# Kernel optimization log

Measured on AMD Instinct MI355X. Metric: run time of the kernel, lower is better.

Reference implementation:

```python
import jax, jax.numpy as jnp
import numpy as np

NUM_HEADS = 8
HEAD_CH = 32  # embed_channels // num_heads = 256 // 8
BN_EPS = 1e-3


def _conv(x, w, pad):
    return jax.lax.conv_general_dilated(
        x, w, window_strides=(1, 1), padding=[(pad, pad), (pad, pad)],
        dimension_numbers=('NCHW', 'OIHW', 'NCHW'))


def _bn(x, gamma, beta):
    # inference BN with running_mean=0, running_var=1 (fresh buffers)
    scale = gamma / jnp.sqrt(1.0 + BN_EPS)
    return x * scale[None, :, None, None] + beta[None, :, None, None]


def setup_inputs() -> dict:
    key = jax.random.key(0)
    ks = jax.random.split(key, 8)
    B, Cin, H, W = 16, 512, 40, 40
    N, Cg, E, Cout = 80, 512, 256, 512
    s = 0.05
    return {
        'x': jax.random.normal(ks[0], (B, Cin, H, W), jnp.float32),
        'guide': jax.random.normal(ks[1], (B, N, Cg), jnp.float32),
        'We': jax.random.normal(ks[2], (E, Cin, 1, 1), jnp.float32) * s,
        'gamma_e': jnp.ones((E,), jnp.float32),
        'beta_e': jnp.zeros((E,), jnp.float32),
        'Wg': jax.random.normal(ks[3], (E, Cg), jnp.float32) * s,
        'bg': jnp.zeros((E,), jnp.float32),
        'head_bias': jnp.zeros((NUM_HEADS,), jnp.float32),
        'Wp': jax.random.normal(ks[4], (Cout, Cin, 3, 3), jnp.float32) * s,
        'gamma_p': jnp.ones((Cout,), jnp.float32),
        'beta_p': jnp.zeros((Cout,), jnp.float32),
    }


def reference(x, guide, We, gamma_e, beta_e, Wg, bg, head_bias, Wp, gamma_p, beta_p):
    B, _, H, W = x.shape
    M, C = NUM_HEADS, HEAD_CH
    # guide_fc: [B, n, Cg] -> [B, n, M, C]
    g = (jnp.einsum('bnc,ec->bne', guide, Wg) + bg).reshape(B, -1, M, C)
    # embed_conv (1x1 + BN, no act): [B, M, C, H, W]
    e = _bn(_conv(x, We, 0), gamma_e, beta_e).reshape(B, M, C, H, W)
    # attention scores, max over guide tokens, scale, bias, sigmoid
    attn = jnp.einsum('bmchw,bnmc->bmhwn', e, g)
    attn = jnp.max(attn, axis=-1) / (C ** 0.5)
    attn = jax.nn.sigmoid(attn + head_bias[None, :, None, None])
    # project_conv (3x3 + BN, no act), gated per head
    p = _bn(_conv(x, Wp, 1), gamma_p, beta_p)
    p = p.reshape(B, M, -1, H, W) * attn[:, :, None, :, :]
    return p.reshape(B, -1, H, W)
```

## Files before the change

kernel.cpp:

```cpp
#include <hip/hip_runtime.h>
#include <hip/hip_bf16.h>
#include <stdint.h>

#define B_   16
#define CIN  512
#define HW   1600
#define E_   256
#define NTOK 80
#define CG   512
#define COUT 512
#define NHEAD 8
#define HCH  32
#define SP   (42*42)

typedef __attribute__((ext_vector_type(8))) short bf16x8;
typedef __attribute__((ext_vector_type(4))) float f32x4;

__device__ __forceinline__ unsigned short f2bf(float f) {
  union { float f; unsigned int i; } v; v.f = f;
  unsigned int x = v.i;
  return (unsigned short)((x + 0x7FFFu + ((x >> 16) & 1u)) >> 16);
}

__global__ void k_prep_x(const float* __restrict__ x, unsigned short* __restrict__ xt) {
  __shared__ float tile[32][33];
  int hw0 = blockIdx.x * 32, ci0 = blockIdx.y * 32, b = blockIdx.z;
  int tx = threadIdx.x, ty = threadIdx.y;
  const float* xp = x + ((size_t)b * CIN + ci0) * HW + hw0;
#pragma unroll
  for (int j = 0; j < 4; j++) tile[ty + 8 * j][tx] = xp[(size_t)(ty + 8 * j) * HW + tx];
  __syncthreads();
  int ci = ci0 + tx;
#pragma unroll
  for (int j = 0; j < 4; j++) {
    int hw = hw0 + ty + 8 * j;
    int h = hw / 40, w = hw - h * 40;
    xt[((size_t)b * SP + (size_t)(h + 1) * 42 + (w + 1)) * CIN + ci] = f2bf(tile[tx][ty + 8 * j]);
  }
}

__global__ void k_prep_wp(const float* __restrict__ Wp, unsigned short* __restrict__ wpb2) {
  int idx = blockIdx.x * 256 + threadIdx.x;
  int co = idx >> 9, ci = idx & 511;
  const float* s = Wp + (size_t)idx * 9;
#pragma unroll
  for (int t = 0; t < 9; t++) wpb2[(size_t)co * (9 * CIN) + t * CIN + ci] = f2bf(s[t]);
}

__global__ void k_cast_all(const float* __restrict__ We, unsigned short* __restrict__ web,
                           const float* __restrict__ Wg, unsigned short* __restrict__ wgb,
                           const float* __restrict__ gu, unsigned short* __restrict__ gub) {
  int i = blockIdx.x * 256 + threadIdx.x;
  const float* src; unsigned short* dst; int j;
  if (i < 32768)       { src = We; dst = web; j = i; }
  else if (i < 65536)  { src = Wg; dst = wgb; j = i - 32768; }
  else                 { src = gu; dst = gub; j = i - 65536; }
  float4 v = ((const float4*)src)[j];
  ushort4 o; o.x = f2bf(v.x); o.y = f2bf(v.y); o.z = f2bf(v.z); o.w = f2bf(v.w);
  ((ushort4*)dst)[j] = o;
}

__global__ __launch_bounds__(512, 2)
void k_fused(const unsigned short* __restrict__ wpb2, const unsigned short* __restrict__ web,
             const unsigned short* __restrict__ wgb,  const unsigned short* __restrict__ xt,
             const unsigned short* __restrict__ gub,
             const float* __restrict__ gamma_e, const float* __restrict__ beta_e,
             const float* __restrict__ gamma_p, const float* __restrict__ beta_p,
             const float* __restrict__ bg,
             float* __restrict__ out, unsigned short* __restrict__ et,
             unsigned short* __restrict__ gbf) {
  __shared__ unsigned short L[3 * 16384];
  char* LB = (char*)L;
  int tid = threadIdx.x;
  int wg = blockIdx.x;

  int role, m0, n0;
  if (wg < 200)      { int w = (wg & 7) * 25 + (wg >> 3);
                       role = 0; m0 = (w / 100) * 256; n0 = (w % 100) * 256; }
  else if (wg < 300) { role = 1; m0 = 0; n0 = (wg - 200) * 256; }
  else               { role = 2; m0 = 0; n0 = (wg - 300) * 256; }

  const int RS    = (role == 0) ? 9 * CIN : CIN;
  const int NSTEP = (role == 0) ? 144 : 16;
  const bool tapjump = (role == 0);
  const unsigned short* Aw = (role == 0) ? wpb2 : (role == 1) ? web : wgb;

  int lane = tid & 63, wid = tid >> 6;
  int wr = wid >> 2, wc = wid & 3;

  int rloc = tid >> 2;
  int kq_g = ((tid & 3) ^ ((tid >> 3) & 3)) * 8;
  const unsigned short* pA = Aw + (size_t)(m0 + rloc) * RS + kq_g;
  const unsigned short* pB0;
  const unsigned short* pB1;
  if (role == 2) {
    pB0 = gub + (size_t)(n0 + rloc) * CIN + kq_g;
    pB1 = pB0 + (size_t)128 * CIN;
  } else {
    int c0 = n0 + rloc, c1 = c0 + 128;
    int b0 = c0 / 1600, hw0 = c0 - b0 * 1600;
    int b1 = c1 / 1600, hw1 = c1 - b1 * 1600;
    int h0 = hw0 / 40, w0 = hw0 - h0 * 40;
    int h1 = hw1 / 40, w1 = hw1 - h1 * 40;
    int ctr = (role == 1) ? 43 : 0;
    pB0 = xt + ((size_t)b0 * SP + h0 * 42 + w0 + ctr) * CIN + kq_g;
    pB1 = xt + ((size_t)b1 * SP + h1 * 42 + w1 + ctr) * CIN + kq_g;
  }

  int scnt = 0;
#define GL(src, dst) __builtin_amdgcn_global_load_lds((const __attribute__((address_space(1))) unsigned int*)(src), \
        (__attribute__((address_space(3))) unsigned int*)(dst), 16, 0, 0)
  auto STG_A = [&](unsigned bo) {
    GL(pA,            LB + bo +     0u + tid * 16u);
    GL(pA + 128 * RS, LB + bo +  8192u + tid * 16u);
  };
  auto STG_B = [&](unsigned bo) {
    GL(pB0,           LB + bo + 16384u + tid * 16u);
    GL(pB1,           LB + bo + 24576u + tid * 16u);
  };
  auto ADV = [&]() {
    pA += 32; pB0 += 32; pB1 += 32;
    if (tapjump) { ++scnt; if ((scnt % 48) == 0) { pB0 += 19968; pB1 += 19968; } }
  };

  int frow = lane & 15;
  int sg = ((lane >> 4) ^ ((frow >> 1) & 3)) << 4;
  int aoff[8], boff[4];
#pragma unroll
  for (int i = 0; i < 8; i++) aoff[i] = (wr * 128 + i * 16 + frow) * 64 + sg;
#pragma unroll
  for (int i = 0; i < 4; i++) boff[i] = 16384 + (wc * 64 + i * 16 + frow) * 64 + sg;

  f32x4 acc[8][4] = {};

  STG_A(0u); STG_B(0u); ADV();
  STG_A(32768u); STG_B(32768u); ADV();
  unsigned r0 = 0u, r1 = 32768u, r2 = 65536u;

  for (int s = 0; s < NSTEP; ++s) {
    if (s + 1 < NSTEP) { asm volatile("s_waitcnt vmcnt(4)" ::: "memory"); }
    else               { asm volatile("s_waitcnt vmcnt(0)" ::: "memory"); }
    __builtin_amdgcn_s_barrier();
    __builtin_amdgcn_sched_barrier(0);
    const char* base = LB + r0;
    bool pre = (s + 2 < NSTEP);
    bf16x8 af[8], bv[4];
#pragma unroll
    for (int i = 0; i < 4; i++) af[i] = *(const bf16x8*)(base + aoff[i]);
#pragma unroll
    for (int i = 0; i < 4; i++) bv[i] = *(const bf16x8*)(base + boff[i]);
    if (pre) STG_A(r2);
    __builtin_amdgcn_s_barrier();
    __builtin_amdgcn_s_setprio(1);
#pragma unroll
    for (int mi = 0; mi < 4; mi++)
#pragma unroll
      for (int ni = 0; ni < 4; ni++)
        acc[mi][ni] = __builtin_amdgcn_mfma_f32_16x16x32_bf16(af[mi], bv[ni], acc[mi][ni], 0, 0, 0);
    __builtin_amdgcn_s_setprio(0);
    __builtin_amdgcn_s_barrier();
#pragma unroll
    for (int i = 4; i < 8; i++) af[i] = *(const bf16x8*)(base + aoff[i]);
    if (pre) { STG_B(r2); ADV(); }
    __builtin_amdgcn_s_barrier();
    __builtin_amdgcn_s_setprio(1);
#pragma unroll
    for (int mi = 4; mi < 8; mi++)
#pragma unroll
      for (int ni = 0; ni < 4; ni++)
        acc[mi][ni] = __builtin_amdgcn_mfma_f32_16x16x32_bf16(af[mi], bv[ni], acc[mi][ni], 0, 0, 0);
    __builtin_amdgcn_s_setprio(0);
    unsigned t = r0; r0 = r1; r1 = r2; r2 = t;
  }
#undef GL

  const float BN_RSQ = 0.9995003746877732f;
  int colb = n0 + wc * 64 + frow;
  int rowb = m0 + wr * 128 + (lane >> 4) * 4;
  if (role == 0) {
#pragma unroll
    for (int mi = 0; mi < 8; mi++) {
      float sc[4], bt[4];
#pragma unroll
      for (int j = 0; j < 4; j++) {
        int co = rowb + mi * 16 + j;
        sc[j] = gamma_p[co] * BN_RSQ; bt[j] = beta_p[co];
      }
#pragma unroll
      for (int ni = 0; ni < 4; ni++) {
        int col = colb + ni * 16;
        int b = col / 1600, hw = col - b * 1600;
#pragma unroll
        for (int j = 0; j < 4; j++) {
          int co = rowb + mi * 16 + j;
          out[((size_t)b * COUT + co) * HW + hw] = acc[mi][ni][j] * sc[j] + bt[j];
        }
      }
    }
  } else if (role == 1) {
#pragma unroll
    for (int mi = 0; mi < 8; mi++) {
      float sc[4], bt[4];
#pragma unroll
      for (int j = 0; j < 4; j++) {
        int ech = rowb + mi * 16 + j;
        sc[j] = gamma_e[ech] * BN_RSQ; bt[j] = beta_e[ech];
      }
#pragma unroll
      for (int ni = 0; ni < 4; ni++) {
        int col = colb + ni * 16;
        int b = col / 1600, hw = col - b * 1600;
        ushort4 pk;
        pk.x = f2bf(acc[mi][ni][0] * sc[0] + bt[0]);
        pk.y = f2bf(acc[mi][ni][1] * sc[1] + bt[1]);
        pk.z = f2bf(acc[mi][ni][2] * sc[2] + bt[2]);
        pk.w = f2bf(acc[mi][ni][3] * sc[3] + bt[3]);
        *(ushort4*)(et + ((size_t)b * HW + hw) * E_ + (rowb + mi * 16)) = pk;
      }
    }
  } else {
#pragma unroll
    for (int mi = 0; mi < 8; mi++) {
      float bt[4];
#pragma unroll
      for (int j = 0; j < 4; j++) bt[j] = bg[rowb + mi * 16 + j];
#pragma unroll
      for (int ni = 0; ni < 4; ni++) {
        int col = colb + ni * 16;
        ushort4 pk;
        pk.x = f2bf(acc[mi][ni][0] + bt[0]);
        pk.y = f2bf(acc[mi][ni][1] + bt[1]);
        pk.z = f2bf(acc[mi][ni][2] + bt[2]);
        pk.w = f2bf(acc[mi][ni][3] + bt[3]);
        *(ushort4*)(gbf + (size_t)col * E_ + (rowb + mi * 16)) = pk;
      }
    }
  }
}

__global__ void k_attn_mfma(const unsigned short* __restrict__ et, const unsigned short* __restrict__ gbf,
                            const float* __restrict__ head_bias, float* __restrict__ attn) {
  __shared__ unsigned short gs[NTOK * HCH];
  int b = blockIdx.z, m = blockIdx.y;
  int tid = threadIdx.x, lane = tid & 63, wid = tid >> 6;
  for (int i = tid; i < NTOK * HCH / 8; i += 256) {
    int n = i >> 2, c = (i & 3) * 8;
    *(bf16x8*)&gs[n * HCH + c] = *(const bf16x8*)&gbf[((size_t)b * NTOK + n) * E_ + m * HCH + c];
  }
  __syncthreads();
  int col = lane & 15, kq = (lane >> 4) * 8;
  bf16x8 bfr[5];
#pragma unroll
  for (int ni = 0; ni < 5; ni++)
    bfr[ni] = *(const bf16x8*)&gs[(ni * 16 + col) * HCH + kq];

  int hw0 = blockIdx.x * 256 + wid * 64;
  bf16x8 afr[4];
#pragma unroll
  for (int mi = 0; mi < 4; mi++) {
    int hw = hw0 + mi * 16 + col; if (hw > HW - 1) hw = HW - 1;
    afr[mi] = *(const bf16x8*)&et[((size_t)b * HW + hw) * E_ + m * HCH + kq];
  }
  float hb = head_bias[m];
  float* attnp = attn + ((size_t)b * NHEAD + m) * HW;
#pragma unroll
  for (int mi = 0; mi < 4; mi++) {
    f32x4 d[5];
#pragma unroll
    for (int ni = 0; ni < 5; ni++) {
      f32x4 z = {0.f, 0.f, 0.f, 0.f};
      d[ni] = __builtin_amdgcn_mfma_f32_16x16x32_bf16(afr[mi], bfr[ni], z, 0, 0, 0);
    }
#pragma unroll
    for (int j = 0; j < 4; j++) {
      float v = fmaxf(fmaxf(fmaxf(d[0][j], d[1][j]), fmaxf(d[2][j], d[3][j])), d[4][j]);
      v = fmaxf(v, __shfl_xor(v, 1, 16));
      v = fmaxf(v, __shfl_xor(v, 2, 16));
      v = fmaxf(v, __shfl_xor(v, 4, 16));
      v = fmaxf(v, __shfl_xor(v, 8, 16));
      if (col == j) {
        int hwout = hw0 + mi * 16 + (lane >> 4) * 4 + j;
        if (hwout < HW)
          attnp[hwout] = 1.0f / (1.0f + __expf(-(v * 0.17677669529663687f + hb)));
      }
    }
  }
}

__global__ void k_gate(float* __restrict__ out, const float* __restrict__ attn) {
  int idx = blockIdx.x * 256 + threadIdx.x;
  int f4 = idx * 4;
  int b = f4 / (COUT * HW);
  int rem = f4 - b * (COUT * HW);
  int co = rem / HW, hw = rem - co * HW;
  float4 a = *(const float4*)(attn + ((size_t)b * NHEAD + (co >> 6)) * HW + hw);
  float4 p = ((float4*)out)[idx];
  p.x *= a.x; p.y *= a.y; p.z *= a.z; p.w *= a.w;
  ((float4*)out)[idx] = p;
}

extern "C" void kernel_launch(void* const* d_in, const int* in_sizes, int n_in,
                              void* d_out, int out_size, void* d_ws, size_t ws_size,
                              hipStream_t stream) {
  const float* x         = (const float*)d_in[0];
  const float* guide     = (const float*)d_in[1];
  const float* We        = (const float*)d_in[2];
  const float* gamma_e   = (const float*)d_in[3];
  const float* beta_e    = (const float*)d_in[4];
  const float* Wg        = (const float*)d_in[5];
  const float* bg        = (const float*)d_in[6];
  const float* head_bias = (const float*)d_in[7];
  const float* Wp        = (const float*)d_in[8];
  const float* gamma_p   = (const float*)d_in[9];
  const float* beta_p    = (const float*)d_in[10];
  float* out = (float*)d_out;

  char* ws = (char*)d_ws;
  size_t off = 0;
  auto alloc = [&](size_t bytes) { char* p = ws + off; off += (bytes + 255) & ~(size_t)255; return p; };
  unsigned short* xt   = (unsigned short*)alloc((size_t)B_ * SP * CIN * 2);
  unsigned short* wpb2 = (unsigned short*)alloc((size_t)COUT * 9 * CIN * 2);
  unsigned short* web  = (unsigned short*)alloc((size_t)E_ * CIN * 2);
  unsigned short* wgb  = (unsigned short*)alloc((size_t)E_ * CG * 2);
  unsigned short* gub  = (unsigned short*)alloc((size_t)B_ * NTOK * CG * 2);
  unsigned short* gbf  = (unsigned short*)alloc((size_t)B_ * NTOK * E_ * 2);
  unsigned short* et   = (unsigned short*)alloc((size_t)B_ * HW * E_ * 2);
  float* attn          = (float*)alloc((size_t)B_ * NHEAD * HW * 4);

  hipMemsetAsync(xt, 0, (size_t)B_ * SP * CIN * 2, stream);
  k_prep_x<<<dim3(50, 16, B_), dim3(32, 8), 0, stream>>>(x, xt);
  k_prep_wp<<<dim3(1024), dim3(256), 0, stream>>>(Wp, wpb2);
  k_cast_all<<<dim3(896), dim3(256), 0, stream>>>(We, web, Wg, wgb, guide, gub);
  k_fused<<<dim3(305), dim3(512), 0, stream>>>(wpb2, web, wgb, xt, gub,
      gamma_e, beta_e, gamma_p, beta_p, bg, out, et, gbf);
  k_attn_mfma<<<dim3(7, NHEAD, B_), dim3(256), 0, stream>>>(et, gbf, head_bias, attn);
  k_gate<<<dim3(12800), dim3(256), 0, stream>>>(out, attn);
}
```

Measured before the change: 302.1 us.

## Split fused GEMM into stages and fuse attention gate into conv epilogue

```diff
diff --git a/kernel.cpp b/kernel.cpp
--- a/kernel.cpp
+++ b/kernel.cpp
@@ -37,14 +37,6 @@
     int h = hw / 40, w = hw - h * 40;
     xt[((size_t)b * SP + (size_t)(h + 1) * 42 + (w + 1)) * CIN + ci] = f2bf(tile[tx][ty + 8 * j]);
   }
-}
-
-__global__ void k_prep_wp(const float* __restrict__ Wp, unsigned short* __restrict__ wpb2) {
-  int idx = blockIdx.x * 256 + threadIdx.x;
-  int co = idx >> 9, ci = idx & 511;
-  const float* s = Wp + (size_t)idx * 9;
-#pragma unroll
-  for (int t = 0; t < 9; t++) wpb2[(size_t)co * (9 * CIN) + t * CIN + ci] = f2bf(s[t]);
 }
 
 __global__ void k_cast_all(const float* __restrict__ We, unsigned short* __restrict__ web,
@@ -60,31 +52,16 @@
   ((ushort4*)dst)[j] = o;
 }
 
-__global__ __launch_bounds__(512, 2)
-void k_fused(const unsigned short* __restrict__ wpb2, const unsigned short* __restrict__ web,
-             const unsigned short* __restrict__ wgb,  const unsigned short* __restrict__ xt,
-             const unsigned short* __restrict__ gub,
-             const float* __restrict__ gamma_e, const float* __restrict__ beta_e,
-             const float* __restrict__ gamma_p, const float* __restrict__ beta_p,
-             const float* __restrict__ bg,
-             float* __restrict__ out, unsigned short* __restrict__ et,
-             unsigned short* __restrict__ gbf) {
-  __shared__ unsigned short L[3 * 16384];
-  char* LB = (char*)L;
+template<int EPI>
+__device__ __forceinline__ void gemm_body(
+    const unsigned short* __restrict__ Aw, const unsigned short* __restrict__ Bx,
+    int m0, int n0,
+    const float* __restrict__ g_sc, const float* __restrict__ g_bt,
+    const float* __restrict__ attn, float* __restrict__ out,
+    unsigned short* __restrict__ ob16, char* LB) {
+  constexpr int RS    = (EPI == 1) ? 9 * CIN : CIN;
+  constexpr int NSTEP = (EPI == 1) ? 144 : 16;
   int tid = threadIdx.x;
-  int wg = blockIdx.x;
-
-  int role, m0, n0;
-  if (wg < 200)      { int w = (wg & 7) * 25 + (wg >> 3);
-                       role = 0; m0 = (w / 100) * 256; n0 = (w % 100) * 256; }
-  else if (wg < 300) { role = 1; m0 = 0; n0 = (wg - 200) * 256; }
-  else               { role = 2; m0 = 0; n0 = (wg - 300) * 256; }
-
-  const int RS    = (role == 0) ? 9 * CIN : CIN;
-  const int NSTEP = (role == 0) ? 144 : 16;
-  const bool tapjump = (role == 0);
-  const unsigned short* Aw = (role == 0) ? wpb2 : (role == 1) ? web : wgb;
-
   int lane = tid & 63, wid = tid >> 6;
   int wr = wid >> 2, wc = wid & 3;
 
@@ -93,8 +70,8 @@
   const unsigned short* pA = Aw + (size_t)(m0 + rloc) * RS + kq_g;
   const unsigned short* pB0;
   const unsigned short* pB1;
-  if (role == 2) {
-    pB0 = gub + (size_t)(n0 + rloc) * CIN + kq_g;
+  if constexpr (EPI == 2) {
+    pB0 = Bx + (size_t)(n0 + rloc) * CIN + kq_g;
     pB1 = pB0 + (size_t)128 * CIN;
   } else {
     int c0 = n0 + rloc, c1 = c0 + 128;
@@ -102,25 +79,24 @@
     int b1 = c1 / 1600, hw1 = c1 - b1 * 1600;
     int h0 = hw0 / 40, w0 = hw0 - h0 * 40;
     int h1 = hw1 / 40, w1 = hw1 - h1 * 40;
-    int ctr = (role == 1) ? 43 : 0;
-    pB0 = xt + ((size_t)b0 * SP + h0 * 42 + w0 + ctr) * CIN + kq_g;
-    pB1 = xt + ((size_t)b1 * SP + h1 * 42 + w1 + ctr) * CIN + kq_g;
+    constexpr int ctr = (EPI == 0) ? 43 : 0;
+    pB0 = Bx + ((size_t)b0 * SP + h0 * 42 + w0 + ctr) * CIN + kq_g;
+    pB1 = Bx + ((size_t)b1 * SP + h1 * 42 + w1 + ctr) * CIN + kq_g;
   }
 
   int scnt = 0;
 #define GL(src, dst) __builtin_amdgcn_global_load_lds((const __attribute__((address_space(1))) unsigned int*)(src), \
         (__attribute__((address_space(3))) unsigned int*)(dst), 16, 0, 0)
-  auto STG_A = [&](unsigned bo) {
+  auto STG = [&](unsigned bo) {
     GL(pA,            LB + bo +     0u + tid * 16u);
     GL(pA + 128 * RS, LB + bo +  8192u + tid * 16u);
-  };
-  auto STG_B = [&](unsigned bo) {
     GL(pB0,           LB + bo + 16384u + tid * 16u);
     GL(pB1,           LB + bo + 24576u + tid * 16u);
-  };
-  auto ADV = [&]() {
     pA += 32; pB0 += 32; pB1 += 32;
-    if (tapjump) { ++scnt; if ((scnt % 48) == 0) { pB0 += 19968; pB1 += 19968; } }
+    if constexpr (EPI == 1) {
+      ++scnt;
+      if ((scnt % 48) == 0) { pB0 += 19968; pB1 += 19968; }
+    }
   };
 
   int frow = lane & 15;
@@ -133,43 +109,61 @@
 
   f32x4 acc[8][4] = {};
 
-  STG_A(0u); STG_B(0u); ADV();
-  STG_A(32768u); STG_B(32768u); ADV();
+  STG(0u); STG(32768u);
   unsigned r0 = 0u, r1 = 32768u, r2 = 65536u;
-
   for (int s = 0; s < NSTEP; ++s) {
     if (s + 1 < NSTEP) { asm volatile("s_waitcnt vmcnt(4)" ::: "memory"); }
     else               { asm volatile("s_waitcnt vmcnt(0)" ::: "memory"); }
     __builtin_amdgcn_s_barrier();
     __builtin_amdgcn_sched_barrier(0);
+    if (s + 2 < NSTEP) STG(r2);
     const char* base = LB + r0;
-    bool pre = (s + 2 < NSTEP);
-    bf16x8 af[8], bv[4];
-#pragma unroll
-    for (int i = 0; i < 4; i++) af[i] = *(const bf16x8*)(base + aoff[i]);
+    bf16x8 bv[4];
 #pragma unroll
     for (int i = 0; i < 4; i++) bv[i] = *(const bf16x8*)(base + boff[i]);
-    if (pre) STG_A(r2);
-    __builtin_amdgcn_s_barrier();
-    __builtin_amdgcn_s_setprio(1);
-#pragma unroll
-    for (int mi = 0; mi < 4; mi++)
-#pragma unroll
-      for (int ni = 0; ni < 4; ni++)
-        acc[mi][ni] = __builtin_amdgcn_mfma_f32_16x16x32_bf16(af[mi], bv[ni], acc[mi][ni], 0, 0, 0);
-    __builtin_amdgcn_s_setprio(0);
-    __builtin_amdgcn_s_barrier();
-#pragma unroll
-    for (int i = 4; i < 8; i++) af[i] = *(const bf16x8*)(base + aoff[i]);
-    if (pre) { STG_B(r2); ADV(); }
-    __builtin_amdgcn_s_barrier();
-    __builtin_amdgcn_s_setprio(1);
-#pragma unroll
-    for (int mi = 4; mi < 8; mi++)
-#pragma unroll
-      for (int ni = 0; ni < 4; ni++)
-        acc[mi][ni] = __builtin_amdgcn_mfma_f32_16x16x32_bf16(af[mi], bv[ni], acc[mi][ni], 0, 0, 0);
-    __builtin_amdgcn_s_setprio(0);
+    if ((wid & 1) == 0) {
+      bf16x8 a0[4];
+#pragma unroll
+      for (int i = 0; i < 4; i++) a0[i] = *(const bf16x8*)(base + aoff[i]);
+      __builtin_amdgcn_s_setprio(1);
+#pragma unroll
+      for (int mi = 0; mi < 4; mi++)
+#pragma unroll
+        for (int ni = 0; ni < 4; ni++)
+          acc[mi][ni] = __builtin_amdgcn_mfma_f32_16x16x32_bf16(a0[mi], bv[ni], acc[mi][ni], 0, 0, 0);
+      __builtin_amdgcn_s_setprio(0);
+      bf16x8 a1[4];
+#pragma unroll
+      for (int i = 0; i < 4; i++) a1[i] = *(const bf16x8*)(base + aoff[4 + i]);
+      __builtin_amdgcn_s_setprio(1);
+#pragma unroll
+      for (int mi = 0; mi < 4; mi++)
+#pragma unroll
+        for (int ni = 0; ni < 4; ni++)
+          acc[4 + mi][ni] = __builtin_amdgcn_mfma_f32_16x16x32_bf16(a1[mi], bv[ni], acc[4 + mi][ni], 0, 0, 0);
+      __builtin_amdgcn_s_setprio(0);
+    } else {
+      bf16x8 a1[4];
+#pragma unroll
+      for (int i = 0; i < 4; i++) a1[i] = *(const bf16x8*)(base + aoff[4 + i]);
+      __builtin_amdgcn_s_setprio(1);
+#pragma unroll
+      for (int mi = 0; mi < 4; mi++)
+#pragma unroll
+        for (int ni = 0; ni < 4; ni++)
+          acc[4 + mi][ni] = __builtin_amdgcn_mfma_f32_16x16x32_bf16(a1[mi], bv[ni], acc[4 + mi][ni], 0, 0, 0);
+      __builtin_amdgcn_s_setprio(0);
+      bf16x8 a0[4];
+#pragma unroll
+      for (int i = 0; i < 4; i++) a0[i] = *(const bf16x8*)(base + aoff[i]);
+      __builtin_amdgcn_s_setprio(1);
+#pragma unroll
+      for (int mi = 0; mi < 4; mi++)
+#pragma unroll
+        for (int ni = 0; ni < 4; ni++)
+          acc[mi][ni] = __builtin_amdgcn_mfma_f32_16x16x32_bf16(a0[mi], bv[ni], acc[mi][ni], 0, 0, 0);
+      __builtin_amdgcn_s_setprio(0);
+    }
     unsigned t = r0; r0 = r1; r1 = r2; r2 = t;
   }
 #undef GL
@@ -177,34 +171,36 @@
   const float BN_RSQ = 0.9995003746877732f;
   int colb = n0 + wc * 64 + frow;
   int rowb = m0 + wr * 128 + (lane >> 4) * 4;
-  if (role == 0) {
+  if constexpr (EPI == 1) {
 #pragma unroll
     for (int mi = 0; mi < 8; mi++) {
+      int head = (m0 + wr * 128 + mi * 16) >> 6;
       float sc[4], bt[4];
 #pragma unroll
       for (int j = 0; j < 4; j++) {
         int co = rowb + mi * 16 + j;
-        sc[j] = gamma_p[co] * BN_RSQ; bt[j] = beta_p[co];
+        sc[j] = g_sc[co] * BN_RSQ; bt[j] = g_bt[co];
       }
 #pragma unroll
       for (int ni = 0; ni < 4; ni++) {
         int col = colb + ni * 16;
         int b = col / 1600, hw = col - b * 1600;
+        float gate = attn[((size_t)b * NHEAD + head) * HW + hw];
 #pragma unroll
         for (int j = 0; j < 4; j++) {
           int co = rowb + mi * 16 + j;
-          out[((size_t)b * COUT + co) * HW + hw] = acc[mi][ni][j] * sc[j] + bt[j];
+          out[((size_t)b * COUT + co) * HW + hw] = (acc[mi][ni][j] * sc[j] + bt[j]) * gate;
         }
       }
     }
-  } else if (role == 1) {
+  } else if constexpr (EPI == 0) {
 #pragma unroll
     for (int mi = 0; mi < 8; mi++) {
       float sc[4], bt[4];
 #pragma unroll
       for (int j = 0; j < 4; j++) {
         int ech = rowb + mi * 16 + j;
-        sc[j] = gamma_e[ech] * BN_RSQ; bt[j] = beta_e[ech];
+        sc[j] = g_sc[ech] * BN_RSQ; bt[j] = g_bt[ech];
       }
 #pragma unroll
       for (int ni = 0; ni < 4; ni++) {
@@ -215,7 +211,7 @@
         pk.y = f2bf(acc[mi][ni][1] * sc[1] + bt[1]);
         pk.z = f2bf(acc[mi][ni][2] * sc[2] + bt[2]);
         pk.w = f2bf(acc[mi][ni][3] * sc[3] + bt[3]);
-        *(ushort4*)(et + ((size_t)b * HW + hw) * E_ + (rowb + mi * 16)) = pk;
+        *(ushort4*)(ob16 + ((size_t)b * HW + hw) * E_ + (rowb + mi * 16)) = pk;
       }
     }
   } else {
@@ -223,7 +219,7 @@
     for (int mi = 0; mi < 8; mi++) {
       float bt[4];
 #pragma unroll
-      for (int j = 0; j < 4; j++) bt[j] = bg[rowb + mi * 16 + j];
+      for (int j = 0; j < 4; j++) bt[j] = g_bt[rowb + mi * 16 + j];
 #pragma unroll
       for (int ni = 0; ni < 4; ni++) {
         int col = colb + ni * 16;
@@ -232,10 +228,45 @@
         pk.y = f2bf(acc[mi][ni][1] + bt[1]);
         pk.z = f2bf(acc[mi][ni][2] + bt[2]);
         pk.w = f2bf(acc[mi][ni][3] + bt[3]);
-        *(ushort4*)(gbf + (size_t)col * E_ + (rowb + mi * 16)) = pk;
-      }
-    }
-  }
+        *(ushort4*)(ob16 + (size_t)col * E_ + (rowb + mi * 16)) = pk;
+      }
+    }
+  }
+}
+
+__global__ __launch_bounds__(512, 1)
+void k_stage1(const unsigned short* __restrict__ web, const unsigned short* __restrict__ wgb,
+              const unsigned short* __restrict__ xt,  const unsigned short* __restrict__ gub,
+              const float* __restrict__ gamma_e, const float* __restrict__ beta_e,
+              const float* __restrict__ bg,
+              unsigned short* __restrict__ et, unsigned short* __restrict__ gbf,
+              const float* __restrict__ Wp, unsigned short* __restrict__ wpb2) {
+  __shared__ unsigned short L[3 * 16384];
+  int wg = blockIdx.x;
+  if (wg < 100) {
+    gemm_body<0>(web, xt, 0, wg * 256, gamma_e, beta_e, nullptr, nullptr, et, (char*)L);
+  } else if (wg < 105) {
+    gemm_body<2>(wgb, gub, 0, (wg - 100) * 256, nullptr, bg, nullptr, nullptr, gbf, (char*)L);
+  } else {
+    int g = (wg - 105) * 512 + threadIdx.x;
+    for (int idx = g; idx < COUT * CIN; idx += 150 * 512) {
+      int co = idx >> 9, ci = idx & 511;
+      const float* s = Wp + (size_t)idx * 9;
+#pragma unroll
+      for (int t = 0; t < 9; t++) wpb2[(size_t)co * (9 * CIN) + t * CIN + ci] = f2bf(s[t]);
+    }
+  }
+}
+
+__global__ __launch_bounds__(512, 1)
+void k_conv3(const unsigned short* __restrict__ wpb2, const unsigned short* __restrict__ xt,
+             const float* __restrict__ gamma_p, const float* __restrict__ beta_p,
+             const float* __restrict__ attn, float* __restrict__ out) {
+  __shared__ unsigned short L[3 * 16384];
+  int wg = blockIdx.x;
+  int w = (wg & 7) * 25 + (wg >> 3);
+  int m0 = (w / 100) * 256, n0 = (w % 100) * 256;
+  gemm_body<1>(wpb2, xt, m0, n0, gamma_p, beta_p, attn, out, nullptr, (char*)L);
 }
 
 __global__ void k_attn_mfma(const unsigned short* __restrict__ et, const unsigned short* __restrict__ gbf,
@@ -285,18 +316,6 @@
       }
     }
   }
-}
-
-__global__ void k_gate(float* __restrict__ out, const float* __restrict__ attn) {
-  int idx = blockIdx.x * 256 + threadIdx.x;
-  int f4 = idx * 4;
-  int b = f4 / (COUT * HW);
-  int rem = f4 - b * (COUT * HW);
-  int co = rem / HW, hw = rem - co * HW;
-  float4 a = *(const float4*)(attn + ((size_t)b * NHEAD + (co >> 6)) * HW + hw);
-  float4 p = ((float4*)out)[idx];
-  p.x *= a.x; p.y *= a.y; p.z *= a.z; p.w *= a.w;
-  ((float4*)out)[idx] = p;
 }
 
 extern "C" void kernel_launch(void* const* d_in, const int* in_sizes, int n_in,
@@ -329,10 +348,8 @@
 
   hipMemsetAsync(xt, 0, (size_t)B_ * SP * CIN * 2, stream);
   k_prep_x<<<dim3(50, 16, B_), dim3(32, 8), 0, stream>>>(x, xt);
-  k_prep_wp<<<dim3(1024), dim3(256), 0, stream>>>(Wp, wpb2);
   k_cast_all<<<dim3(896), dim3(256), 0, stream>>>(We, web, Wg, wgb, guide, gub);
-  k_fused<<<dim3(305), dim3(512), 0, stream>>>(wpb2, web, wgb, xt, gub,
-      gamma_e, beta_e, gamma_p, beta_p, bg, out, et, gbf);
+  k_stage1<<<dim3(255), dim3(512), 0, stream>>>(web, wgb, xt, gub, gamma_e, beta_e, bg, et, gbf, Wp, wpb2);
   k_attn_mfma<<<dim3(7, NHEAD, B_), dim3(256), 0, stream>>>(et, gbf, head_bias, attn);
-  k_gate<<<dim3(12800), dim3(256), 0, stream>>>(out, attn);
-}
+  k_conv3<<<dim3(200), dim3(512), 0, stream>>>(wpb2, xt, gamma_p, beta_p, attn, out);
+}
```

Measured after the change: 304.8 us. About the same (+0.9%).
